# Optimization experiments

Measured on AMD Instinct MI355X. Metric: run time of the kernel, lower is better.

## Reference

```python
import jax, jax.numpy as jnp
import numpy as np
from jax import lax

WINDOW_SIZE = 11
SIGMA = 1.5
DATA_RANGE = 1.0
EPS = 1e-8


def _gauss_1d(window_size=WINDOW_SIZE, sigma=SIGMA):
    coords = jnp.arange(window_size, dtype=jnp.float32) - window_size // 2
    g = jnp.exp(-(coords ** 2) / (2.0 * sigma ** 2))
    return g / g.sum()


def _gaussian_filter(x, w1d):
    # Separable depthwise blur: horizontal then vertical, VALID padding (use_padding=False).
    C = x.shape[1]
    win = w1d.shape[0]
    kh = jnp.broadcast_to(w1d.reshape(1, 1, 1, win), (C, 1, 1, win))  # OIHW, groups=C
    kv = jnp.broadcast_to(w1d.reshape(1, 1, win, 1), (C, 1, win, 1))
    dn = ('NCHW', 'OIHW', 'NCHW')
    out = lax.conv_general_dilated(x, kh, (1, 1), 'VALID',
                                   dimension_numbers=dn, feature_group_count=C)
    out = lax.conv_general_dilated(out, kv, (1, 1), 'VALID',
                                   dimension_numbers=dn, feature_group_count=C)
    return out


def setup_inputs() -> dict:
    key = jax.random.key(0)
    k1, k2 = jax.random.split(key)
    B, C, H, W = 16, 3, 768, 768
    X = jax.random.uniform(k1, (B, C, H, W), dtype=jnp.float32)
    Y = jax.random.uniform(k2, (B, C, H, W), dtype=jnp.float32)
    window = _gauss_1d()
    return {"X": X, "Y": Y, "window": window}


def reference(X, Y, window):
    K1, K2 = 0.01, 0.03
    C1 = (K1 * DATA_RANGE) ** 2
    C2 = (K2 * DATA_RANGE) ** 2
    mu_x = _gaussian_filter(X, window)
    mu_y = _gaussian_filter(Y, window)
    sigma_x = _gaussian_filter(X * X, window) - mu_x ** 2
    sigma_y = _gaussian_filter(Y * Y, window) - mu_y ** 2
    sigma_xy = _gaussian_filter(X * Y, window) - mu_x * mu_y
    cs = (2.0 * sigma_xy + C2) / (sigma_x + sigma_y + C2 + EPS)
    cs = jax.nn.relu(cs)
    ssim_map = (2.0 * mu_x * mu_y + C1) / (mu_x ** 2 + mu_y ** 2 + C1 + EPS) * cs
    ssim_val = ssim_map.mean(axis=(1, 2, 3))  # [B]
    return ssim_val
```

## Files before the change

### kernel.cpp

```cpp
#include <hip/hip_runtime.h>


#define H_IMG 768
#define W_IMG 768
#define OH 758
#define OW_TOT 758
#define OWS 256
#define NSEG 16

__global__ void ssim_zero_out(float* __restrict__ out) {
    if (threadIdx.x < 16) out[threadIdx.x] = 0.0f;
}

__attribute__((amdgpu_flat_work_group_size(256, 256), amdgpu_waves_per_eu(3, 3)))
__global__ void ssim_fused(const float* __restrict__ X, const float* __restrict__ Y,
                           const float* __restrict__ Wg, float* __restrict__ out) {
    const float C1 = 1e-4f, C2 = 9e-4f, EPS = 1e-8f;
    const float INV_COUNT = 1.0f / (3.0f * 758.0f * 758.0f);

    const int t = threadIdx.x;
    int bx = blockIdx.x;
    const int seg = bx & (NSEG - 1); bx >>= 4;
    const int strip = bx % 3; bx /= 3;
    const int ch = bx % 3;
    const int b  = bx / 3;

    const int R0 = (OH * seg) / NSEG;
    const int Rend = (OH * (seg + 1)) / NSEG;
    const int hseg = Rend - R0;
    const int c0 = strip * OWS;

    const float* Xi = X + (size_t)(b * 3 + ch) * (H_IMG * W_IMG);
    const float* Yi = Y + (size_t)(b * 3 + ch) * (H_IMG * W_IMG);

    float w[11];
#pragma unroll
    for (int k = 0; k < 11; ++k) w[k] = Wg[k];

    __shared__ float hb[4][4][OWS];
    __shared__ float red[4];

    const int sA = t >> 6;
    const int cg = t & 63;
    const int colbase = c0 + 4 * cg;
    const int k0 = min(colbase,      W_IMG - 4);
    const int k1 = min(colbase + 4,  W_IMG - 4);
    const int k2 = min(colbase + 8,  W_IMG - 4);
    const int k3 = min(colbase + 12, W_IMG - 2);

    float rg[4][16];
#pragma unroll
    for (int f = 0; f < 4; ++f)
#pragma unroll
        for (int j = 0; j < 16; ++j) rg[f][j] = 0.0f;

    const bool colok = (c0 + t) < OW_TOT;
    float local = 0.0f;
    const int M = (hseg + 13) >> 2;

    for (int mb = 0; mb < M; mb += 4) {
#pragma unroll
        for (int p = 0; p < 4; ++p) {
            const int m = mb + p;
            if (m < M) {
                {
                    int r = R0 + 4 * m + sA;
                    r = min(r, H_IMG - 1);
                    const float* xr = Xi + (size_t)r * W_IMG;
                    const float* yr = Yi + (size_t)r * W_IMG;
                    float4 xa = *(const float4*)(xr + k0);
                    float4 xb = *(const float4*)(xr + k1);
                    float4 xc = *(const float4*)(xr + k2);
                    float2 xd = *(const float2*)(xr + k3);
                    float4 ya = *(const float4*)(yr + k0);
                    float4 yb = *(const float4*)(yr + k1);
                    float4 yc = *(const float4*)(yr + k2);
                    float2 yd = *(const float2*)(yr + k3);
                    float xv[14] = {xa.x, xa.y, xa.z, xa.w, xb.x, xb.y, xb.z, xb.w,
                                    xc.x, xc.y, xc.z, xc.w, xd.x, xd.y};
                    float yv[14] = {ya.x, ya.y, ya.z, ya.w, yb.x, yb.y, yb.z, yb.w,
                                    yc.x, yc.y, yc.z, yc.w, yd.x, yd.y};
                    float sv[14], pv[14];
#pragma unroll
                    for (int j = 0; j < 14; ++j) {
                        pv[j] = xv[j] * yv[j];
                        sv[j] = fmaf(xv[j], xv[j], yv[j] * yv[j]);
                    }
                    float h0[4], h1[4], h2[4], h3[4];
#pragma unroll
                    for (int cc = 0; cc < 4; ++cc) {
                        float a0 = 0.f, a1 = 0.f, a2 = 0.f, a3 = 0.f;
#pragma unroll
                        for (int k = 0; k < 11; ++k) {
                            a0 = fmaf(w[k], xv[cc + k], a0);
                            a1 = fmaf(w[k], yv[cc + k], a1);
                            a2 = fmaf(w[k], sv[cc + k], a2);
                            a3 = fmaf(w[k], pv[cc + k], a3);
                        }
                        h0[cc] = a0; h1[cc] = a1; h2[cc] = a2; h3[cc] = a3;
                    }
                    *(float4*)&hb[sA][0][4 * cg] = make_float4(h0[0], h0[1], h0[2], h0[3]);
                    *(float4*)&hb[sA][1][4 * cg] = make_float4(h1[0], h1[1], h1[2], h1[3]);
                    *(float4*)&hb[sA][2][4 * cg] = make_float4(h2[0], h2[1], h2[2], h2[3]);
                    *(float4*)&hb[sA][3][4 * cg] = make_float4(h3[0], h3[1], h3[2], h3[3]);
                }
                __syncthreads();

                {
#pragma unroll
                    for (int s2 = 0; s2 < 4; ++s2) {
#pragma unroll
                        for (int f = 0; f < 4; ++f)
                            rg[f][(4 * p + s2) & 15] = hb[s2][f][t];
                    }
#pragma unroll
                    for (int s2 = 0; s2 < 4; ++s2) {
                        const int orel = 4 * m - 10 + s2;
                        float a0 = 0.f, a1 = 0.f, a2 = 0.f, a3 = 0.f;
#pragma unroll
                        for (int k = 0; k < 11; ++k) {
                            const int sl = (4 * p + s2 + k + 6) & 15;
                            a0 = fmaf(w[k], rg[0][sl], a0);
                            a1 = fmaf(w[k], rg[1][sl], a1);
                            a2 = fmaf(w[k], rg[2][sl], a2);
                            a3 = fmaf(w[k], rg[3][sl], a3);
                        }
                        const float mux2 = a0 * a0;
                        const float muy2 = a1 * a1;
                        const float mxy  = a0 * a1;
                        const float sigsum = a2 - mux2 - muy2;
                        const float sxy    = a3 - mxy;
                        const float num = (2.0f * mxy + C1) * (2.0f * sxy + C2);
                        const float den = (mux2 + muy2 + C1 + EPS) * (sigsum + C2 + EPS);
                        const float v = fmaxf(__fdividef(num, den), 0.0f);
                        if (colok && (orel >= 0) && (orel < hseg)) local += v;
                    }
                }
                __syncthreads();
            }
        }
    }

    float v = local;
#pragma unroll
    for (int off = 32; off > 0; off >>= 1) v += __shfl_down(v, off, 64);
    if ((t & 63) == 0) red[t >> 6] = v;
    __syncthreads();
    if (t == 0) {
        atomicAdd(&out[b], (red[0] + red[1] + red[2] + red[3]) * INV_COUNT);
    }
}

extern "C" void kernel_launch(void* const* d_in, const int* in_sizes, int n_in,
                              void* d_out, int out_size, void* d_ws, size_t ws_size,
                              hipStream_t stream) {
    const float* X  = (const float*)d_in[0];
    const float* Y  = (const float*)d_in[1];
    const float* Wg = (const float*)d_in[2];
    float* out = (float*)d_out;

    hipLaunchKernelGGL(ssim_zero_out, dim3(1), dim3(64), 0, stream, out);
    hipLaunchKernelGGL(ssim_fused, dim3(16 * 3 * 3 * NSEG), dim3(256), 0, stream,
                       X, Y, Wg, out);
}
```

Baseline: 325.8 us.

## Shrink blocks to single 64-wide wavefront strips with interleaved LDS layout

Each block now covers a 64-column strip with one wavefront (12 strips instead of 3), so there are four times as many smaller blocks. A block-wide barrier costs less with a single wave, and the final LDS reduction step disappears. The horizontal-pass results are stored interleaved as float4 per column, so the vertical pass reads all four fields with one LDS load. The x²+y² computation now reuses the xv registers to lower register pressure. In exchange, the 10-column halo is re-read for every 64 output columns, which raises redundant global loads and horizontal-pass work, and there are more atomics.

Result: slower. 362.5 us (+11.3%).

```diff
diff --git a/kernel.cpp b/kernel.cpp
--- a/kernel.cpp
+++ b/kernel.cpp
@@ -5,14 +5,15 @@
 #define W_IMG 768
 #define OH 758
 #define OW_TOT 758
-#define OWS 256
+#define OWS 64
+#define NSTRIP 12
 #define NSEG 16
 
 __global__ void ssim_zero_out(float* __restrict__ out) {
     if (threadIdx.x < 16) out[threadIdx.x] = 0.0f;
 }
 
-__attribute__((amdgpu_flat_work_group_size(256, 256), amdgpu_waves_per_eu(3, 3)))
+__attribute__((amdgpu_flat_work_group_size(64, 64), amdgpu_waves_per_eu(4, 8)))
 __global__ void ssim_fused(const float* __restrict__ X, const float* __restrict__ Y,
                            const float* __restrict__ Wg, float* __restrict__ out) {
     const float C1 = 1e-4f, C2 = 9e-4f, EPS = 1e-8f;
@@ -20,8 +21,8 @@
 
     const int t = threadIdx.x;
     int bx = blockIdx.x;
+    const int strip = bx % NSTRIP; bx /= NSTRIP;
     const int seg = bx & (NSEG - 1); bx >>= 4;
-    const int strip = bx % 3; bx /= 3;
     const int ch = bx % 3;
     const int b  = bx / 3;
 
@@ -37,11 +38,10 @@
 #pragma unroll
     for (int k = 0; k < 11; ++k) w[k] = Wg[k];
 
-    __shared__ float hb[4][4][OWS];
-    __shared__ float red[4];
+    __shared__ __align__(16) float hb[4][OWS][4];
 
-    const int sA = t >> 6;
-    const int cg = t & 63;
+    const int sA = t >> 4;
+    const int cg = t & 15;
     const int colbase = c0 + 4 * cg;
     const int k0 = min(colbase,      W_IMG - 4);
     const int k1 = min(colbase + 4,  W_IMG - 4);
@@ -80,38 +80,49 @@
                                     xc.x, xc.y, xc.z, xc.w, xd.x, xd.y};
                     float yv[14] = {ya.x, ya.y, ya.z, ya.w, yb.x, yb.y, yb.z, yb.w,
                                     yc.x, yc.y, yc.z, yc.w, yd.x, yd.y};
-                    float sv[14], pv[14];
+                    float pv[14];
 #pragma unroll
-                    for (int j = 0; j < 14; ++j) {
-                        pv[j] = xv[j] * yv[j];
-                        sv[j] = fmaf(xv[j], xv[j], yv[j] * yv[j]);
-                    }
-                    float h0[4], h1[4], h2[4], h3[4];
+                    for (int j = 0; j < 14; ++j) pv[j] = xv[j] * yv[j];
+
+                    float h0[4], h1[4], h3[4];
 #pragma unroll
                     for (int cc = 0; cc < 4; ++cc) {
-                        float a0 = 0.f, a1 = 0.f, a2 = 0.f, a3 = 0.f;
+                        float a0 = 0.f, a1 = 0.f, a3 = 0.f;
 #pragma unroll
                         for (int k = 0; k < 11; ++k) {
                             a0 = fmaf(w[k], xv[cc + k], a0);
                             a1 = fmaf(w[k], yv[cc + k], a1);
-                            a2 = fmaf(w[k], sv[cc + k], a2);
                             a3 = fmaf(w[k], pv[cc + k], a3);
                         }
-                        h0[cc] = a0; h1[cc] = a1; h2[cc] = a2; h3[cc] = a3;
+                        h0[cc] = a0; h1[cc] = a1; h3[cc] = a3;
                     }
-                    *(float4*)&hb[sA][0][4 * cg] = make_float4(h0[0], h0[1], h0[2], h0[3]);
-                    *(float4*)&hb[sA][1][4 * cg] = make_float4(h1[0], h1[1], h1[2], h1[3]);
-                    *(float4*)&hb[sA][2][4 * cg] = make_float4(h2[0], h2[1], h2[2], h2[3]);
-                    *(float4*)&hb[sA][3][4 * cg] = make_float4(h3[0], h3[1], h3[2], h3[3]);
+#pragma unroll
+                    for (int j = 0; j < 14; ++j)
+                        xv[j] = fmaf(xv[j], xv[j], yv[j] * yv[j]);
+                    float h2[4];
+#pragma unroll
+                    for (int cc = 0; cc < 4; ++cc) {
+                        float a2 = 0.f;
+#pragma unroll
+                        for (int k = 0; k < 11; ++k)
+                            a2 = fmaf(w[k], xv[cc + k], a2);
+                        h2[cc] = a2;
+                    }
+#pragma unroll
+                    for (int cc = 0; cc < 4; ++cc) {
+                        *(float4*)&hb[sA][4 * cg + cc][0] =
+                            make_float4(h0[cc], h1[cc], h2[cc], h3[cc]);
+                    }
                 }
                 __syncthreads();
 
                 {
 #pragma unroll
                     for (int s2 = 0; s2 < 4; ++s2) {
-#pragma unroll
-                        for (int f = 0; f < 4; ++f)
-                            rg[f][(4 * p + s2) & 15] = hb[s2][f][t];
+                        float4 hv = *(const float4*)&hb[s2][t][0];
+                        const int sl = (4 * p + s2) & 15;
+                        rg[0][sl] = hv.x; rg[1][sl] = hv.y;
+                        rg[2][sl] = hv.z; rg[3][sl] = hv.w;
                     }
 #pragma unroll
                     for (int s2 = 0; s2 < 4; ++s2) {
@@ -144,11 +155,7 @@
     float v = local;
 #pragma unroll
     for (int off = 32; off > 0; off >>= 1) v += __shfl_down(v, off, 64);
-    if ((t & 63) == 0) red[t >> 6] = v;
-    __syncthreads();
-    if (t == 0) {
-        atomicAdd(&out[b], (red[0] + red[1] + red[2] + red[3]) * INV_COUNT);
-    }
+    if (t == 0) atomicAdd(&out[b], v * INV_COUNT);
 }
 
 extern "C" void kernel_launch(void* const* d_in, const int* in_sizes, int n_in,
@@ -160,6 +167,6 @@
     float* out = (float*)d_out;
 
     hipLaunchKernelGGL(ssim_zero_out, dim3(1), dim3(64), 0, stream, out);
-    hipLaunchKernelGGL(ssim_fused, dim3(16 * 3 * 3 * NSEG), dim3(256), 0, stream,
+    hipLaunchKernelGGL(ssim_fused, dim3(48 * NSEG * NSTRIP), dim3(64), 0, stream,
                        X, Y, Wg, out);
 }
```
